# Kernel optimization log

Hardware: AMD Instinct MI355X
Metric: run time of the kernel (lower is better)

## Reference

```python
import jax, jax.numpy as jnp
import numpy as np

NEG = -9e15  # fill value used by the torch module for invalid band locations


def _sliding_window_attention(q, k, v, w, padding_mask):
    """Banded (Longformer-style) attention.
    q, k, v: [B, H, S, d]; padding_mask: [B, S] (nonzero = valid).
    S must be a multiple of 2*w (matches the no-extra-padding path of the
    original module). Returns context [B, H, S, d].
    """
    B, H, S, d = q.shape
    nb = S // w  # number of query blocks of size w
    # Query blocks: [B, H, nb, w, d]
    q_c = q.reshape(B, H, nb, w, d)
    # Each query block attends to a 3w-wide key/value slab (w halo each side).
    idx = (jnp.arange(nb) * w)[:, None] + jnp.arange(3 * w)[None, :]  # [nb, 3w]
    k_pad = jnp.pad(k, ((0, 0), (0, 0), (w, w), (0, 0)))
    v_pad = jnp.pad(v, ((0, 0), (0, 0), (w, w), (0, 0)))
    k_c = k_pad[:, :, idx, :]  # [B, H, nb, 3w, d]
    v_c = v_pad[:, :, idx, :]  # [B, H, nb, 3w, d]
    # Block scores: [B, H, nb, w, 3w]
    scores3 = jnp.einsum('bhnxd,bhnyd->bhnxy', q_c, k_c)
    # Extract the (2w+1)-wide band: query local x, band offset j -> slab col x+j
    x_idx = jnp.arange(w)[:, None]                     # [w, 1]
    j_idx = x_idx + jnp.arange(2 * w + 1)[None, :]     # [w, 2w+1], values in [0, 3w-1]
    band = scores3[..., x_idx, j_idx]                  # [B, H, nb, w, 2w+1]
    # Validity: global key position i - w + j must lie in [0, S) and be unpadded.
    key_pos = jnp.arange(S).reshape(nb, w)[:, :, None] - w + jnp.arange(2 * w + 1)
    valid = (key_pos >= 0) & (key_pos < S)                       # [nb, w, 2w+1]
    kmask = padding_mask[:, jnp.clip(key_pos, 0, S - 1)] != 0    # [B, nb, w, 2w+1]
    m = valid[None, None] & kmask[:, None]                       # [B, H, nb, w, 2w+1]
    band = jnp.where(m, band, NEG)
    # Original scales by sqrt(q.shape[-1]) == sqrt(head_dim)
    attn = jax.nn.softmax(band / jnp.sqrt(jnp.asarray(d, band.dtype)), axis=-1)
    attn = jnp.where(m, attn, 0.0)  # mirrors the explicit softmax_mask zeroing
    # Scatter band back to slab layout and contract with values.
    attn3 = jnp.zeros_like(scores3).at[..., x_idx, j_idx].set(attn)
    ctx = jnp.einsum('bhnxy,bhnyd->bhnxd', attn3, v_c)
    return ctx.reshape(B, H, S, d)


def setup_inputs() -> dict:
    key = jax.random.key(0)
    k0, k1, k2 = jax.random.split(key, 3)
    B, S, D, E = 2, 4096, 1024, 1024
    x = jax.random.normal(k0, (B, S, D), jnp.float32)
    padding_mask = jnp.ones((B, S), jnp.int32)
    # xavier_uniform like the torch _reset_parameters; biases zero
    s_qkv = (6.0 / (D + 3 * E)) ** 0.5
    Wqkv = jax.random.uniform(k1, (3 * E, D), jnp.float32, -s_qkv, s_qkv)
    bqkv = jnp.zeros((3 * E,), jnp.float32)
    s_o = (6.0 / (E + E)) ** 0.5
    Wo = jax.random.uniform(k2, (E, E), jnp.float32, -s_o, s_o)
    bo = jnp.zeros((E,), jnp.float32)
    return {'x': x, 'padding_mask': padding_mask, 'Wqkv': Wqkv, 'bqkv': bqkv,
            'Wo': Wo, 'bo': bo}


def reference(x, padding_mask, Wqkv, bqkv, Wo, bo):
    B, S, D = x.shape
    E = Wo.shape[0]
    H = 16
    hd = E // H
    w = 512 // 2  # window_size // 2
    qkv = (x @ Wqkv.T + bqkv).reshape(B, S, H, 3, hd)
    q = jnp.transpose(qkv[..., 0, :], (0, 2, 1, 3))  # [B, H, S, hd]
    k = jnp.transpose(qkv[..., 1, :], (0, 2, 1, 3))
    v = jnp.transpose(qkv[..., 2, :], (0, 2, 1, 3))
    ctx = _sliding_window_attention(q, k, v, w, padding_mask)
    out = jnp.transpose(ctx, (0, 2, 1, 3)).reshape(B, S, E)
    return out @ Wo.T + bo
```

## Files before the change

kernel.cpp:

```cpp
#include <hip/hip_runtime.h>
#include <hip/hip_bf16.h>
#include <stdint.h>

typedef __attribute__((ext_vector_type(8))) short short8;
typedef __attribute__((ext_vector_type(4))) float f32x4;

#define QSCALE 0.18033688011112042f

__device__ __forceinline__ unsigned short f2bf(float f) {
  unsigned int u = __builtin_bit_cast(unsigned int, f);
  u += 0x7FFFu + ((u >> 16) & 1u);
  return (unsigned short)(u >> 16);
}

__device__ __forceinline__ unsigned short f2bf_fast(float f) {
  __hip_bfloat16 h = __float2bfloat16(f);
  return __builtin_bit_cast(unsigned short, h);
}

__device__ __forceinline__ float exp2_fast(float x) {
  float r; asm("v_exp_f32 %0, %1" : "=v"(r) : "v"(x)); return r;
}

#define GLD_LDS16(gp, lp) \
  __builtin_amdgcn_global_load_lds((const __attribute__((address_space(1))) void*)(gp), \
                                   (__attribute__((address_space(3))) void*)(lp), 16, 0, 0)

__global__ __launch_bounds__(256) void cvt_all_kernel(
    const float* __restrict__ x, const float* __restrict__ Wqkv, const float* __restrict__ Wo,
    unsigned short* __restrict__ xb, unsigned short* __restrict__ Wqkvb,
    unsigned short* __restrict__ Wob) {
  int i = blockIdx.x * 256 + threadIdx.x;
  const float* src; unsigned short* dst; int local; float scale = 1.0f;
  if (i < 1048576) { src = x; dst = xb; local = i; }
  else if (i < 1048576 + 393216) {
    local = i - 1048576; src = Wqkv; dst = Wqkvb;
    int row = (local * 8) >> 10;
    if (((row >> 6) % 3) == 0) scale = QSCALE;
  } else { local = i - 1441792; src = Wo; dst = Wob; }
  const float4* s4 = (const float4*)src;
  float4 a = s4[local * 2], b = s4[local * 2 + 1];
  uint4 o;
  o.x = (unsigned)f2bf(a.x * scale) | ((unsigned)f2bf(a.y * scale) << 16);
  o.y = (unsigned)f2bf(a.z * scale) | ((unsigned)f2bf(a.w * scale) << 16);
  o.z = (unsigned)f2bf(b.x * scale) | ((unsigned)f2bf(b.y * scale) << 16);
  o.w = (unsigned)f2bf(b.z * scale) | ((unsigned)f2bf(b.w * scale) << 16);
  *(uint4*)(dst + (size_t)local * 8) = o;
}

template<int EPI>
__global__ __launch_bounds__(256, 4) void gemm_bt(
    const unsigned short* __restrict__ A, const unsigned short* __restrict__ Bw,
    const float* __restrict__ bias, void* o0, void* o1, void* o2,
    int M, int N, int K, int nbc)
{
  __shared__ __align__(16) unsigned short Asm[128 * 64];
  __shared__ __align__(16) unsigned short Bsm[128 * 64];
  int bid = blockIdx.x;
  int bc = bid % nbc, br = bid / nbc;
  int tid = threadIdx.x;
  int lane = tid & 63, w = tid >> 6;
  int l16 = lane & 15, g = lane >> 4;
  int wr = w >> 1, wc = w & 1;
  f32x4 acc[4][4];
  #pragma unroll
  for (int i = 0; i < 4; i++)
    #pragma unroll
    for (int j = 0; j < 4; j++) acc[i][j] = (f32x4){0.f, 0.f, 0.f, 0.f};

  const int nkt = K >> 6;
  for (int kt = 0; kt < nkt; ++kt) {
    __syncthreads();
    #pragma unroll
    for (int r = 0; r < 4; ++r) {
      int idx = tid + 256 * r;
      int row = idx >> 3, s = idx & 7;
      int gofs = ((s ^ (row & 7)) << 3) + (kt << 6);
      GLD_LDS16(A + (size_t)(br * 128 + row) * K + gofs, &Asm[idx << 3]);
      GLD_LDS16(Bw + (size_t)(bc * 128 + row) * K + gofs, &Bsm[idx << 3]);
    }
    __syncthreads();
    #pragma unroll
    for (int kk = 0; kk < 2; ++kk) {
      short8 af[4], bf[4];
      #pragma unroll
      for (int i = 0; i < 4; i++) {
        int rowa = wr * 64 + i * 16 + l16;
        af[i] = *(const short8*)&Asm[(rowa << 6) + ((((kk << 2) + g) ^ (rowa & 7)) << 3)];
        int rowb = wc * 64 + i * 16 + l16;
        bf[i] = *(const short8*)&Bsm[(rowb << 6) + ((((kk << 2) + g) ^ (rowb & 7)) << 3)];
      }
      #pragma unroll
      for (int i = 0; i < 4; i++)
        #pragma unroll
        for (int j = 0; j < 4; j++)
          acc[i][j] = __builtin_amdgcn_mfma_f32_16x16x32_bf16(af[i], bf[j], acc[i][j], 0, 0, 0);
    }
  }
  #pragma unroll
  for (int i = 0; i < 4; i++) {
    #pragma unroll
    for (int j = 0; j < 4; j++) {
      int n = bc * 128 + wc * 64 + j * 16 + l16;
      int m0 = br * 128 + wr * 64 + i * 16 + g * 4;
      if (EPI == 0) {
        int t = (n >> 6) % 3;
        int hh = n / 192, e = n & 63;
        float bval = bias[n]; if (t == 0) bval *= QSCALE;
        int bb = m0 >> 12, s0 = m0 & 4095;
        if (t == 2) {
          unsigned short p0 = f2bf(acc[i][j][0] + bval);
          unsigned short p1 = f2bf(acc[i][j][1] + bval);
          unsigned short p2 = f2bf(acc[i][j][2] + bval);
          unsigned short p3 = f2bf(acc[i][j][3] + bval);
          uint2 pk;
          pk.x = (unsigned)p0 | ((unsigned)p1 << 16);
          pk.y = (unsigned)p2 | ((unsigned)p3 << 16);
          unsigned short* vt = (unsigned short*)o2;
          *(uint2*)&vt[(((size_t)(bb * 16 + hh) * 64 + e) << 12) + s0] = pk;
        } else {
          unsigned short* dst = (unsigned short*)(t == 0 ? o0 : o1);
          #pragma unroll
          for (int jj = 0; jj < 4; jj++)
            dst[((((size_t)(bb * 16 + hh) << 12) + s0 + jj) << 6) + e] = f2bf(acc[i][j][jj] + bval);
        }
      } else {
        float* o = (float*)o0;
        float bval = bias[n];
        #pragma unroll
        for (int jj = 0; jj < 4; jj++)
          o[(size_t)(m0 + jj) * N + n] = acc[i][j][jj] + bval;
      }
    }
  }
}

__global__ __launch_bounds__(512, 4) void attn_kernel(
    const unsigned short* __restrict__ qb, const unsigned short* __restrict__ kb,
    const unsigned short* __restrict__ vtb, const int* __restrict__ pmask,
    unsigned short* __restrict__ ctxb)
{
  const int S = 4096, HD = 64, WIN = 256;
  const float NEG = -1e38f;
  __shared__ __align__(16) unsigned short Ks[2][64 * 64];
  __shared__ __align__(16) unsigned short Vts[2][64 * 64];
  __shared__ __align__(16) unsigned short Ps[8][16 * 64];

  int bid0 = blockIdx.x;
  int bid = (bid0 & 7) * (gridDim.x >> 3) + (bid0 >> 3);
  int qt = bid & 31;
  int bh = bid >> 5;
  int b = bh >> 4, h = bh & 15;

  const unsigned short* Q  = qb + (size_t)bh * S * HD;
  const unsigned short* Kg = kb + (size_t)bh * S * HD;
  const unsigned short* Vt = vtb + (size_t)bh * HD * S;
  const int* pmrow = pmask + (size_t)b * S;

  int tid = threadIdx.x;
  int lane = tid & 63, w = tid >> 6;
  int l16 = lane & 15, g = lane >> 4;

  int q0 = qt * 128;
  int Q0 = q0 + w * 16;

  short8 qf[2];
  #pragma unroll
  for (int hh = 0; hh < 2; ++hh)
    qf[hh] = *(const short8*)&Q[(size_t)(Q0 + l16) * HD + hh * 32 + g * 8];

  f32x4 ctx[4];
  #pragma unroll
  for (int dt = 0; dt < 4; ++dt) ctx[dt] = (f32x4){0.f, 0.f, 0.f, 0.f};
  float lrun[4] = {0.f, 0.f, 0.f, 0.f};

  int kt0 = (q0 - WIN) >> 6; if (kt0 < 0) kt0 = 0;
  int kt1 = (q0 + 127 + WIN) >> 6; if (kt1 > 63) kt1 = 63;
  int nt = kt1 - kt0 + 1;

#define STAGE(BUF, KT) do {                                                       \
    int kb_ = (KT) * 64;                                                          \
    int row_ = tid >> 3, s_ = tid & 7;                                            \
    int c_ = (s_ ^ (row_ & 7)) << 3;                                              \
    GLD_LDS16(Kg + (size_t)(kb_ + row_) * HD + c_, &Ks[BUF][tid << 3]);           \
    GLD_LDS16(Vt + (size_t)row_ * S + kb_ + c_, &Vts[BUF][tid << 3]);             \
  } while (0)

  STAGE(0, kt0);
  asm volatile("s_waitcnt vmcnt(0)" ::: "memory");
  __syncthreads();

  int cur = 0;
  for (int it = 0; it < nt; ++it) {
    int kbase = (kt0 + it) * 64;
    if (it + 1 < nt) STAGE(cur ^ 1, kt0 + it + 1);

    bool need = (kbase >= Q0 - 319) && (kbase <= Q0 + 271);

    if (need) {
      unsigned long long bm = __ballot(pmrow[kbase + lane] != 0);
      bool allv = (~bm == 0ULL);
      bool full = (kbase >= Q0 - 241) && (kbase <= Q0 + 193);

      f32x4 sc[4];
      __builtin_amdgcn_s_setprio(1);
      #pragma unroll
      for (int k4 = 0; k4 < 4; ++k4) {
        int krow = k4 * 16 + l16;
        f32x4 s = (f32x4){0.f, 0.f, 0.f, 0.f};
        short8 kf0 = *(const short8*)&Ks[cur][(krow << 6) + ((g ^ (l16 & 7)) << 3)];
        s = __builtin_amdgcn_mfma_f32_16x16x32_bf16(qf[0], kf0, s, 0, 0, 0);
        short8 kf1 = *(const short8*)&Ks[cur][(krow << 6) + (((4 + g) ^ (l16 & 7)) << 3)];
        s = __builtin_amdgcn_mfma_f32_16x16x32_bf16(qf[1], kf1, s, 0, 0, 0);
        sc[k4] = s;
      }
      __builtin_amdgcn_s_setprio(0);

      int qbase = Q0 + g * 4;
      if (!full) {
        #pragma unroll
        for (int k4 = 0; k4 < 4; ++k4) {
          int kg = kbase + k4 * 16 + l16;
          #pragma unroll
          for (int jj = 0; jj < 4; ++jj) {
            int dq = kg - (qbase + jj) + WIN;
            sc[k4][jj] = ((unsigned)dq <= 2u * WIN) ? sc[k4][jj] : NEG;
          }
        }
      }
      #pragma unroll
      for (int k4 = 0; k4 < 4; ++k4) {
        int col = k4 * 16 + l16;
        unsigned bit = (unsigned)(bm >> col) & 1u;
        #pragma unroll
        for (int jj = 0; jj < 4; ++jj) {
          float p = exp2_fast(sc[k4][jj]);
          if (!allv) p = bit ? p : 0.f;
          lrun[jj] += p;
          int row = g * 4 + jj;
          Ps[w][(row << 6) + ((((col >> 3) ^ (row & 7)) << 3) | (col & 7))] = f2bf_fast(p);
        }
      }

      asm volatile("s_waitcnt lgkmcnt(0)" ::: "memory");
      __builtin_amdgcn_sched_barrier(0);
      short8 pf0 = *(const short8*)&Ps[w][(l16 << 6) + ((g ^ (l16 & 7)) << 3)];
      short8 pf1 = *(const short8*)&Ps[w][(l16 << 6) + (((4 + g) ^ (l16 & 7)) << 3)];
      __builtin_amdgcn_s_setprio(1);
      #pragma unroll
      for (int dt = 0; dt < 4; ++dt) {
        int drow = dt * 16 + l16;
        short8 vf0 = *(const short8*)&Vts[cur][(drow << 6) + ((g ^ (drow & 7)) << 3)];
        ctx[dt] = __builtin_amdgcn_mfma_f32_16x16x32_bf16(pf0, vf0, ctx[dt], 0, 0, 0);
        short8 vf1 = *(const short8*)&Vts[cur][(drow << 6) + (((4 + g) ^ (drow & 7)) << 3)];
        ctx[dt] = __builtin_amdgcn_mfma_f32_16x16x32_bf16(pf1, vf1, ctx[dt], 0, 0, 0);
      }
      __builtin_amdgcn_s_setprio(0);
    }

    if (it + 1 < nt) {
      asm volatile("s_waitcnt vmcnt(0)" ::: "memory");
      __syncthreads();
      cur ^= 1;
    }
  }
#undef STAGE

  #pragma unroll
  for (int jj = 0; jj < 4; ++jj) {
    float ps = lrun[jj];
    #pragma unroll
    for (int mk = 1; mk < 16; mk <<= 1) ps += __shfl_xor(ps, mk);
    float rc = (ps > 0.f) ? (1.f / ps) : 0.f;
    int qrow = Q0 + g * 4 + jj;
    size_t base = ((size_t)b * S + qrow) * 1024 + h * 64;
    #pragma unroll
    for (int dt = 0; dt < 4; ++dt)
      ctxb[base + dt * 16 + l16] = f2bf(ctx[dt][jj] * rc);
  }
}

extern "C" void kernel_launch(void* const* d_in, const int* in_sizes, int n_in,
                              void* d_out, int out_size, void* d_ws, size_t ws_size,
                              hipStream_t stream) {
  const float* x     = (const float*)d_in[0];
  const int*   pmask = (const int*)d_in[1];
  const float* Wqkv  = (const float*)d_in[2];
  const float* bqkv  = (const float*)d_in[3];
  const float* Wo    = (const float*)d_in[4];
  const float* bo    = (const float*)d_in[5];

  char* wsp = (char*)d_ws;
  unsigned short* xb    = (unsigned short*)(wsp);
  unsigned short* Wqkvb = (unsigned short*)(wsp + (size_t)(16u << 20));
  unsigned short* Wob   = (unsigned short*)(wsp + (size_t)(22u << 20));
  unsigned short* vtb   = (unsigned short*)(wsp + (size_t)(24u << 20));
  unsigned short* ctxb  = (unsigned short*)(wsp + (size_t)(40u << 20));
  unsigned short* qbuf  = (unsigned short*)d_out;
  unsigned short* kbuf  = (unsigned short*)d_out + (size_t)8388608;

  cvt_all_kernel<<<6144, 256, 0, stream>>>(x, Wqkv, Wo, xb, Wqkvb, Wob);

  gemm_bt<0><<<(8192 / 128) * (3072 / 128), 256, 0, stream>>>(
      xb, Wqkvb, bqkv, qbuf, kbuf, vtb, 8192, 3072, 1024, 3072 / 128);

  attn_kernel<<<1024, 512, 0, stream>>>(qbuf, kbuf, vtb, pmask, ctxb);

  gemm_bt<1><<<(8192 / 128) * (1024 / 128), 256, 0, stream>>>(
      ctxb, Wob, bo, d_out, nullptr, nullptr, 8192, 1024, 1024, 1024 / 128);
}
```

Before: 141.7 us.

## Switch attention kernel to 32x32x16 MFMA with 32-row query tiles per wave

Attention now runs 4 waves of 32 query rows each, not 8 waves of 16, and uses 32x32x16 bf16 MFMAs for QK^T and PV instead of 16x16x32. The intent is to raise MFMA efficiency and cut LDS fragment reads per FLOP, since each K/V fragment now serves twice as many query rows. The trade-offs are more accumulator and row-sum registers (16 rows per lane), 256-thread blocks with more staging loads per thread, and coarser band skipping, so more fully masked work is computed per wave.

```diff
diff --git a/kernel.cpp b/kernel.cpp
--- a/kernel.cpp
+++ b/kernel.cpp
@@ -4,6 +4,7 @@
 
 typedef __attribute__((ext_vector_type(8))) short short8;
 typedef __attribute__((ext_vector_type(4))) float f32x4;
+typedef __attribute__((ext_vector_type(16))) float f32x16;
 
 #define QSCALE 0.18033688011112042f
 
@@ -135,16 +136,16 @@
   }
 }
 
-__global__ __launch_bounds__(512, 4) void attn_kernel(
+__global__ __launch_bounds__(256, 3) void attn_kernel(
     const unsigned short* __restrict__ qb, const unsigned short* __restrict__ kb,
     const unsigned short* __restrict__ vtb, const int* __restrict__ pmask,
     unsigned short* __restrict__ ctxb)
 {
-  const int S = 4096, HD = 64, WIN = 256;
+  const int S = 4096, WIN = 256;
   const float NEG = -1e38f;
   __shared__ __align__(16) unsigned short Ks[2][64 * 64];
   __shared__ __align__(16) unsigned short Vts[2][64 * 64];
-  __shared__ __align__(16) unsigned short Ps[8][16 * 64];
+  __shared__ __align__(16) unsigned short Ps[4][32 * 64];
 
   int bid0 = blockIdx.x;
   int bid = (bid0 & 7) * (gridDim.x >> 3) + (bid0 >> 3);
@@ -152,27 +153,27 @@
   int bh = bid >> 5;
   int b = bh >> 4, h = bh & 15;
 
-  const unsigned short* Q  = qb + (size_t)bh * S * HD;
-  const unsigned short* Kg = kb + (size_t)bh * S * HD;
-  const unsigned short* Vt = vtb + (size_t)bh * HD * S;
+  const unsigned short* Q  = qb + (size_t)bh * S * 64;
+  const unsigned short* Kg = kb + (size_t)bh * S * 64;
+  const unsigned short* Vt = vtb + (size_t)bh * 64 * S;
   const int* pmrow = pmask + (size_t)b * S;
 
   int tid = threadIdx.x;
   int lane = tid & 63, w = tid >> 6;
-  int l16 = lane & 15, g = lane >> 4;
+  int l32 = lane & 31, h2 = lane >> 5;
 
   int q0 = qt * 128;
-  int Q0 = q0 + w * 16;
-
-  short8 qf[2];
-  #pragma unroll
-  for (int hh = 0; hh < 2; ++hh)
-    qf[hh] = *(const short8*)&Q[(size_t)(Q0 + l16) * HD + hh * 32 + g * 8];
-
-  f32x4 ctx[4];
-  #pragma unroll
-  for (int dt = 0; dt < 4; ++dt) ctx[dt] = (f32x4){0.f, 0.f, 0.f, 0.f};
-  float lrun[4] = {0.f, 0.f, 0.f, 0.f};
+  int Q0 = q0 + w * 32;
+
+  short8 qf[4];
+  #pragma unroll
+  for (int c = 0; c < 4; ++c)
+    qf[c] = *(const short8*)&Q[(size_t)(Q0 + l32) * 64 + c * 16 + h2 * 8];
+
+  f32x16 ctx0 = (f32x16)(0.f), ctx1 = (f32x16)(0.f);
+  float lrun[16];
+  #pragma unroll
+  for (int r = 0; r < 16; ++r) lrun[r] = 0.f;
 
   int kt0 = (q0 - WIN) >> 6; if (kt0 < 0) kt0 = 0;
   int kt1 = (q0 + 127 + WIN) >> 6; if (kt1 > 63) kt1 = 63;
@@ -180,10 +181,14 @@
 
 #define STAGE(BUF, KT) do {                                                       \
     int kb_ = (KT) * 64;                                                          \
-    int row_ = tid >> 3, s_ = tid & 7;                                            \
-    int c_ = (s_ ^ (row_ & 7)) << 3;                                              \
-    GLD_LDS16(Kg + (size_t)(kb_ + row_) * HD + c_, &Ks[BUF][tid << 3]);           \
-    GLD_LDS16(Vt + (size_t)row_ * S + kb_ + c_, &Vts[BUF][tid << 3]);             \
+    _Pragma("unroll")                                                             \
+    for (int r_ = 0; r_ < 2; ++r_) {                                              \
+      int idx_ = tid + 256 * r_;                                                  \
+      int row_ = idx_ >> 3, s_ = idx_ & 7;                                        \
+      int c_ = (s_ ^ (row_ & 7)) << 3;                                            \
+      GLD_LDS16(Kg + (size_t)(kb_ + row_) * 64 + c_, &Ks[BUF][idx_ << 3]);        \
+      GLD_LDS16(Vt + (size_t)row_ * S + kb_ + c_, &Vts[BUF][idx_ << 3]);          \
+    }                                                                             \
   } while (0)
 
   STAGE(0, kt0);
@@ -195,65 +200,63 @@
     int kbase = (kt0 + it) * 64;
     if (it + 1 < nt) STAGE(cur ^ 1, kt0 + it + 1);
 
-    bool need = (kbase >= Q0 - 319) && (kbase <= Q0 + 271);
-
+    bool need = (kbase >= Q0 - 319) && (kbase <= Q0 + 287);
     if (need) {
       unsigned long long bm = __ballot(pmrow[kbase + lane] != 0);
       bool allv = (~bm == 0ULL);
-      bool full = (kbase >= Q0 - 241) && (kbase <= Q0 + 193);
-
-      f32x4 sc[4];
+      bool full = (kbase >= Q0 - 225) && (kbase <= Q0 + 193);
+
+      f32x16 sc0 = (f32x16)(0.f), sc1 = (f32x16)(0.f);
+      int krow0 = l32, krow1 = 32 + l32;
       __builtin_amdgcn_s_setprio(1);
       #pragma unroll
-      for (int k4 = 0; k4 < 4; ++k4) {
-        int krow = k4 * 16 + l16;
-        f32x4 s = (f32x4){0.f, 0.f, 0.f, 0.f};
-        short8 kf0 = *(const short8*)&Ks[cur][(krow << 6) + ((g ^ (l16 & 7)) << 3)];
-        s = __builtin_amdgcn_mfma_f32_16x16x32_bf16(qf[0], kf0, s, 0, 0, 0);
-        short8 kf1 = *(const short8*)&Ks[cur][(krow << 6) + (((4 + g) ^ (l16 & 7)) << 3)];
-        s = __builtin_amdgcn_mfma_f32_16x16x32_bf16(qf[1], kf1, s, 0, 0, 0);
-        sc[k4] = s;
+      for (int c = 0; c < 4; ++c) {
+        int slot = c * 2 + h2;
+        short8 kf0 = *(const short8*)&Ks[cur][(krow0 << 6) + ((slot ^ (krow0 & 7)) << 3)];
+        sc0 = __builtin_amdgcn_mfma_f32_32x32x16_bf16(qf[c], kf0, sc0, 0, 0, 0);
+        short8 kf1 = *(const short8*)&Ks[cur][(krow1 << 6) + ((slot ^ (krow1 & 7)) << 3)];
+        sc1 = __builtin_amdgcn_mfma_f32_32x32x16_bf16(qf[c], kf1, sc1, 0, 0, 0);
       }
       __builtin_amdgcn_s_setprio(0);
 
-      int qbase = Q0 + g * 4;
+      int col0 = l32, col1 = 32 + l32;
       if (!full) {
         #pragma unroll
-        for (int k4 = 0; k4 < 4; ++k4) {
-          int kg = kbase + k4 * 16 + l16;
-          #pragma unroll
-          for (int jj = 0; jj < 4; ++jj) {
-            int dq = kg - (qbase + jj) + WIN;
-            sc[k4][jj] = ((unsigned)dq <= 2u * WIN) ? sc[k4][jj] : NEG;
-          }
+        for (int r = 0; r < 16; ++r) {
+          int row = (r & 3) + 8 * (r >> 2) + 4 * h2;
+          int d0 = kbase + col0 - (Q0 + row) + WIN;
+          sc0[r] = ((unsigned)d0 <= 2u * WIN) ? sc0[r] : NEG;
+          int d1 = kbase + col1 - (Q0 + row) + WIN;
+          sc1[r] = ((unsigned)d1 <= 2u * WIN) ? sc1[r] : NEG;
         }
       }
-      #pragma unroll
-      for (int k4 = 0; k4 < 4; ++k4) {
-        int col = k4 * 16 + l16;
-        unsigned bit = (unsigned)(bm >> col) & 1u;
-        #pragma unroll
-        for (int jj = 0; jj < 4; ++jj) {
-          float p = exp2_fast(sc[k4][jj]);
-          if (!allv) p = bit ? p : 0.f;
-          lrun[jj] += p;
-          int row = g * 4 + jj;
-          Ps[w][(row << 6) + ((((col >> 3) ^ (row & 7)) << 3) | (col & 7))] = f2bf_fast(p);
-        }
+      unsigned bit0 = (unsigned)(bm >> col0) & 1u;
+      unsigned bit1 = (unsigned)(bm >> col1) & 1u;
+      #pragma unroll
+      for (int r = 0; r < 16; ++r) {
+        int row = (r & 3) + 8 * (r >> 2) + 4 * h2;
+        float p0 = exp2_fast(sc0[r]);
+        float p1 = exp2_fast(sc1[r]);
+        if (!allv) { p0 = bit0 ? p0 : 0.f; p1 = bit1 ? p1 : 0.f; }
+        lrun[r] += p0 + p1;
+        int rb = (row << 6), rx = (row & 7);
+        Ps[w][rb + ((((col0 >> 3) ^ rx) << 3) | (col0 & 7))] = f2bf_fast(p0);
+        Ps[w][rb + ((((col1 >> 3) ^ rx) << 3) | (col1 & 7))] = f2bf_fast(p1);
       }
 
       asm volatile("s_waitcnt lgkmcnt(0)" ::: "memory");
       __builtin_amdgcn_sched_barrier(0);
-      short8 pf0 = *(const short8*)&Ps[w][(l16 << 6) + ((g ^ (l16 & 7)) << 3)];
-      short8 pf1 = *(const short8*)&Ps[w][(l16 << 6) + (((4 + g) ^ (l16 & 7)) << 3)];
+
       __builtin_amdgcn_s_setprio(1);
       #pragma unroll
-      for (int dt = 0; dt < 4; ++dt) {
-        int drow = dt * 16 + l16;
-        short8 vf0 = *(const short8*)&Vts[cur][(drow << 6) + ((g ^ (drow & 7)) << 3)];
-        ctx[dt] = __builtin_amdgcn_mfma_f32_16x16x32_bf16(pf0, vf0, ctx[dt], 0, 0, 0);
-        short8 vf1 = *(const short8*)&Vts[cur][(drow << 6) + (((4 + g) ^ (drow & 7)) << 3)];
-        ctx[dt] = __builtin_amdgcn_mfma_f32_16x16x32_bf16(pf1, vf1, ctx[dt], 0, 0, 0);
+      for (int c = 0; c < 4; ++c) {
+        int slot = c * 2 + h2;
+        short8 pf = *(const short8*)&Ps[w][(l32 << 6) + ((slot ^ (l32 & 7)) << 3)];
+        int dr0 = l32, dr1 = 32 + l32;
+        short8 vf0 = *(const short8*)&Vts[cur][(dr0 << 6) + ((slot ^ (dr0 & 7)) << 3)];
+        ctx0 = __builtin_amdgcn_mfma_f32_32x32x16_bf16(pf, vf0, ctx0, 0, 0, 0);
+        short8 vf1 = *(const short8*)&Vts[cur][(dr1 << 6) + ((slot ^ (dr1 & 7)) << 3)];
+        ctx1 = __builtin_amdgcn_mfma_f32_32x32x16_bf16(pf, vf1, ctx1, 0, 0, 0);
       }
       __builtin_amdgcn_s_setprio(0);
     }
@@ -267,16 +270,19 @@
 #undef STAGE
 
   #pragma unroll
-  for (int jj = 0; jj < 4; ++jj) {
-    float ps = lrun[jj];
-    #pragma unroll
-    for (int mk = 1; mk < 16; mk <<= 1) ps += __shfl_xor(ps, mk);
-    float rc = (ps > 0.f) ? (1.f / ps) : 0.f;
-    int qrow = Q0 + g * 4 + jj;
+  for (int r = 0; r < 16; ++r) {
+    float ps = lrun[r];
+    #pragma unroll
+    for (int mk = 1; mk < 32; mk <<= 1) ps += __shfl_xor(ps, mk);
+    lrun[r] = (ps > 0.f) ? (1.f / ps) : 0.f;
+  }
+  #pragma unroll
+  for (int r = 0; r < 16; ++r) {
+    int row = (r & 3) + 8 * (r >> 2) + 4 * h2;
+    int qrow = Q0 + row;
     size_t base = ((size_t)b * S + qrow) * 1024 + h * 64;
-    #pragma unroll
-    for (int dt = 0; dt < 4; ++dt)
-      ctxb[base + dt * 16 + l16] = f2bf(ctx[dt][jj] * rc);
+    ctxb[base + l32]      = f2bf(ctx0[r] * lrun[r]);
+    ctxb[base + 32 + l32] = f2bf(ctx1[r] * lrun[r]);
   }
 }
 
@@ -304,7 +310,7 @@
   gemm_bt<0><<<(8192 / 128) * (3072 / 128), 256, 0, stream>>>(
       xb, Wqkvb, bqkv, qbuf, kbuf, vtb, 8192, 3072, 1024, 3072 / 128);
 
-  attn_kernel<<<1024, 512, 0, stream>>>(qbuf, kbuf, vtb, pmask, ctxb);
+  attn_kernel<<<1024, 256, 0, stream>>>(qbuf, kbuf, vtb, pmask, ctxb);
 
   gemm_bt<1><<<(8192 / 128) * (1024 / 128), 256, 0, stream>>>(
       ctxb, Wob, bo, d_out, nullptr, nullptr, 8192, 1024, 1024, 1024 / 128);
```

Result: slower. 157.2 us (+10.9%).

## Give each attention wave two query sub-tiles to reuse K/V fragments

Applied to the files above, without the earlier changes.

The attention kernel moves from 8 waves per block with 16 query rows each to 4 waves per block with 32 query rows each (two 16-row sub-tiles). Each K and V fragment read from LDS now feeds two MFMAs, which halves LDS reads per FLOP. The masking and exp pass is fused into the QK loop per k4 chunk, and K/V staging is split across two loads per thread. The cost is more registers per wave and fewer waves per block to hide latency, and the wider query span means some tiles are computed that one sub-tile does not need.

```diff
diff --git a/kernel.cpp b/kernel.cpp
--- a/kernel.cpp
+++ b/kernel.cpp
@@ -135,16 +135,16 @@
   }
 }
 
-__global__ __launch_bounds__(512, 4) void attn_kernel(
+__global__ __launch_bounds__(256, 4) void attn_kernel(
     const unsigned short* __restrict__ qb, const unsigned short* __restrict__ kb,
     const unsigned short* __restrict__ vtb, const int* __restrict__ pmask,
     unsigned short* __restrict__ ctxb)
 {
-  const int S = 4096, HD = 64, WIN = 256;
+  const int S = 4096, WIN = 256;
   const float NEG = -1e38f;
   __shared__ __align__(16) unsigned short Ks[2][64 * 64];
   __shared__ __align__(16) unsigned short Vts[2][64 * 64];
-  __shared__ __align__(16) unsigned short Ps[8][16 * 64];
+  __shared__ __align__(16) unsigned short Ps[4][2][16 * 64];
 
   int bid0 = blockIdx.x;
   int bid = (bid0 & 7) * (gridDim.x >> 3) + (bid0 >> 3);
@@ -152,9 +152,9 @@
   int bh = bid >> 5;
   int b = bh >> 4, h = bh & 15;
 
-  const unsigned short* Q  = qb + (size_t)bh * S * HD;
-  const unsigned short* Kg = kb + (size_t)bh * S * HD;
-  const unsigned short* Vt = vtb + (size_t)bh * HD * S;
+  const unsigned short* Q  = qb + (size_t)bh * S * 64;
+  const unsigned short* Kg = kb + (size_t)bh * S * 64;
+  const unsigned short* Vt = vtb + (size_t)bh * 64 * S;
   const int* pmrow = pmask + (size_t)b * S;
 
   int tid = threadIdx.x;
@@ -162,17 +162,21 @@
   int l16 = lane & 15, g = lane >> 4;
 
   int q0 = qt * 128;
-  int Q0 = q0 + w * 16;
-
-  short8 qf[2];
-  #pragma unroll
-  for (int hh = 0; hh < 2; ++hh)
-    qf[hh] = *(const short8*)&Q[(size_t)(Q0 + l16) * HD + hh * 32 + g * 8];
-
-  f32x4 ctx[4];
-  #pragma unroll
-  for (int dt = 0; dt < 4; ++dt) ctx[dt] = (f32x4){0.f, 0.f, 0.f, 0.f};
-  float lrun[4] = {0.f, 0.f, 0.f, 0.f};
+  int Q0 = q0 + w * 32;
+
+  short8 qf[2][2];
+  #pragma unroll
+  for (int qs = 0; qs < 2; ++qs)
+    #pragma unroll
+    for (int hh = 0; hh < 2; ++hh)
+      qf[qs][hh] = *(const short8*)&Q[(size_t)(Q0 + qs * 16 + l16) * 64 + hh * 32 + g * 8];
+
+  f32x4 ctx[2][4];
+  #pragma unroll
+  for (int qs = 0; qs < 2; ++qs)
+    #pragma unroll
+    for (int dt = 0; dt < 4; ++dt) ctx[qs][dt] = (f32x4){0.f, 0.f, 0.f, 0.f};
+  float lrun[2][4] = {{0.f,0.f,0.f,0.f},{0.f,0.f,0.f,0.f}};
 
   int kt0 = (q0 - WIN) >> 6; if (kt0 < 0) kt0 = 0;
   int kt1 = (q0 + 127 + WIN) >> 6; if (kt1 > 63) kt1 = 63;
@@ -180,10 +184,14 @@
 
 #define STAGE(BUF, KT) do {                                                       \
     int kb_ = (KT) * 64;                                                          \
-    int row_ = tid >> 3, s_ = tid & 7;                                            \
-    int c_ = (s_ ^ (row_ & 7)) << 3;                                              \
-    GLD_LDS16(Kg + (size_t)(kb_ + row_) * HD + c_, &Ks[BUF][tid << 3]);           \
-    GLD_LDS16(Vt + (size_t)row_ * S + kb_ + c_, &Vts[BUF][tid << 3]);             \
+    _Pragma("unroll")                                                             \
+    for (int r_ = 0; r_ < 2; ++r_) {                                              \
+      int idx_ = tid + 256 * r_;                                                  \
+      int row_ = idx_ >> 3, s_ = idx_ & 7;                                        \
+      int c_ = (s_ ^ (row_ & 7)) << 3;                                            \
+      GLD_LDS16(Kg + (size_t)(kb_ + row_) * 64 + c_, &Ks[BUF][idx_ << 3]);        \
+      GLD_LDS16(Vt + (size_t)row_ * S + kb_ + c_, &Vts[BUF][idx_ << 3]);          \
+    }                                                                             \
   } while (0)
 
   STAGE(0, kt0);
@@ -195,65 +203,76 @@
     int kbase = (kt0 + it) * 64;
     if (it + 1 < nt) STAGE(cur ^ 1, kt0 + it + 1);
 
-    bool need = (kbase >= Q0 - 319) && (kbase <= Q0 + 271);
-
+    bool need = (kbase >= Q0 - 319) && (kbase <= Q0 + 287);
     if (need) {
       unsigned long long bm = __ballot(pmrow[kbase + lane] != 0);
       bool allv = (~bm == 0ULL);
-      bool full = (kbase >= Q0 - 241) && (kbase <= Q0 + 193);
-
-      f32x4 sc[4];
+      bool full0 = (kbase >= Q0 - 241) && (kbase <= Q0 + 193);
+      bool full1 = (kbase >= Q0 - 225) && (kbase <= Q0 + 209);
+
       __builtin_amdgcn_s_setprio(1);
       #pragma unroll
       for (int k4 = 0; k4 < 4; ++k4) {
         int krow = k4 * 16 + l16;
-        f32x4 s = (f32x4){0.f, 0.f, 0.f, 0.f};
         short8 kf0 = *(const short8*)&Ks[cur][(krow << 6) + ((g ^ (l16 & 7)) << 3)];
-        s = __builtin_amdgcn_mfma_f32_16x16x32_bf16(qf[0], kf0, s, 0, 0, 0);
+        f32x4 s0 = __builtin_amdgcn_mfma_f32_16x16x32_bf16(qf[0][0], kf0,
+                     (f32x4){0.f, 0.f, 0.f, 0.f}, 0, 0, 0);
+        f32x4 s1 = __builtin_amdgcn_mfma_f32_16x16x32_bf16(qf[1][0], kf0,
+                     (f32x4){0.f, 0.f, 0.f, 0.f}, 0, 0, 0);
         short8 kf1 = *(const short8*)&Ks[cur][(krow << 6) + (((4 + g) ^ (l16 & 7)) << 3)];
-        s = __builtin_amdgcn_mfma_f32_16x16x32_bf16(qf[1], kf1, s, 0, 0, 0);
-        sc[k4] = s;
-      }
-      __builtin_amdgcn_s_setprio(0);
-
-      int qbase = Q0 + g * 4;
-      if (!full) {
+        s0 = __builtin_amdgcn_mfma_f32_16x16x32_bf16(qf[0][1], kf1, s0, 0, 0, 0);
+        s1 = __builtin_amdgcn_mfma_f32_16x16x32_bf16(qf[1][1], kf1, s1, 0, 0, 0);
+
+        int col = k4 * 16 + l16;
+        int kg = kbase + col;
+        unsigned bit = (unsigned)(bm >> col) & 1u;
         #pragma unroll
-        for (int k4 = 0; k4 < 4; ++k4) {
-          int kg = kbase + k4 * 16 + l16;
-          #pragma unroll
-          for (int jj = 0; jj < 4; ++jj) {
-            int dq = kg - (qbase + jj) + WIN;
-            sc[k4][jj] = ((unsigned)dq <= 2u * WIN) ? sc[k4][jj] : NEG;
+        for (int jj = 0; jj < 4; ++jj) {
+          int row = g * 4 + jj;
+          int pofs = (row << 6) + ((((col >> 3) ^ (row & 7)) << 3) | (col & 7));
+          {
+            float sv = s0[jj];
+            if (!full0) {
+              int dq = kg - (Q0 + row) + WIN;
+              sv = ((unsigned)dq <= 2u * WIN) ? sv : NEG;
+            }
+            float p = exp2_fast(sv);
+            if (!allv) p = bit ? p : 0.f;
+            lrun[0][jj] += p;
+            Ps[w][0][pofs] = f2bf_fast(p);
+          }
+          {
+            float sv = s1[jj];
+            if (!full1) {
+              int dq = kg - (Q0 + 16 + row) + WIN;
+              sv = ((unsigned)dq <= 2u * WIN) ? sv : NEG;
+            }
+            float p = exp2_fast(sv);
+            if (!allv) p = bit ? p : 0.f;
+            lrun[1][jj] += p;
+            Ps[w][1][pofs] = f2bf_fast(p);
           }
         }
       }
-      #pragma unroll
-      for (int k4 = 0; k4 < 4; ++k4) {
-        int col = k4 * 16 + l16;
-        unsigned bit = (unsigned)(bm >> col) & 1u;
-        #pragma unroll
-        for (int jj = 0; jj < 4; ++jj) {
-          float p = exp2_fast(sc[k4][jj]);
-          if (!allv) p = bit ? p : 0.f;
-          lrun[jj] += p;
-          int row = g * 4 + jj;
-          Ps[w][(row << 6) + ((((col >> 3) ^ (row & 7)) << 3) | (col & 7))] = f2bf_fast(p);
-        }
-      }
+      __builtin_amdgcn_s_setprio(0);
 
       asm volatile("s_waitcnt lgkmcnt(0)" ::: "memory");
       __builtin_amdgcn_sched_barrier(0);
-      short8 pf0 = *(const short8*)&Ps[w][(l16 << 6) + ((g ^ (l16 & 7)) << 3)];
-      short8 pf1 = *(const short8*)&Ps[w][(l16 << 6) + (((4 + g) ^ (l16 & 7)) << 3)];
+
+      short8 pf00 = *(const short8*)&Ps[w][0][(l16 << 6) + ((g ^ (l16 & 7)) << 3)];
+      short8 pf01 = *(const short8*)&Ps[w][0][(l16 << 6) + (((4 + g) ^ (l16 & 7)) << 3)];
+      short8 pf10 = *(const short8*)&Ps[w][1][(l16 << 6) + ((g ^ (l16 & 7)) << 3)];
+      short8 pf11 = *(const short8*)&Ps[w][1][(l16 << 6) + (((4 + g) ^ (l16 & 7)) << 3)];
       __builtin_amdgcn_s_setprio(1);
       #pragma unroll
       for (int dt = 0; dt < 4; ++dt) {
         int drow = dt * 16 + l16;
         short8 vf0 = *(const short8*)&Vts[cur][(drow << 6) + ((g ^ (drow & 7)) << 3)];
-        ctx[dt] = __builtin_amdgcn_mfma_f32_16x16x32_bf16(pf0, vf0, ctx[dt], 0, 0, 0);
+        ctx[0][dt] = __builtin_amdgcn_mfma_f32_16x16x32_bf16(pf00, vf0, ctx[0][dt], 0, 0, 0);
+        ctx[1][dt] = __builtin_amdgcn_mfma_f32_16x16x32_bf16(pf10, vf0, ctx[1][dt], 0, 0, 0);
         short8 vf1 = *(const short8*)&Vts[cur][(drow << 6) + (((4 + g) ^ (drow & 7)) << 3)];
-        ctx[dt] = __builtin_amdgcn_mfma_f32_16x16x32_bf16(pf1, vf1, ctx[dt], 0, 0, 0);
+        ctx[0][dt] = __builtin_amdgcn_mfma_f32_16x16x32_bf16(pf01, vf1, ctx[0][dt], 0, 0, 0);
+        ctx[1][dt] = __builtin_amdgcn_mfma_f32_16x16x32_bf16(pf11, vf1, ctx[1][dt], 0, 0, 0);
       }
       __builtin_amdgcn_s_setprio(0);
     }
@@ -267,16 +286,19 @@
 #undef STAGE
 
   #pragma unroll
-  for (int jj = 0; jj < 4; ++jj) {
-    float ps = lrun[jj];
-    #pragma unroll
-    for (int mk = 1; mk < 16; mk <<= 1) ps += __shfl_xor(ps, mk);
-    float rc = (ps > 0.f) ? (1.f / ps) : 0.f;
-    int qrow = Q0 + g * 4 + jj;
-    size_t base = ((size_t)b * S + qrow) * 1024 + h * 64;
-    #pragma unroll
-    for (int dt = 0; dt < 4; ++dt)
-      ctxb[base + dt * 16 + l16] = f2bf(ctx[dt][jj] * rc);
+  for (int qs = 0; qs < 2; ++qs) {
+    #pragma unroll
+    for (int jj = 0; jj < 4; ++jj) {
+      float ps = lrun[qs][jj];
+      #pragma unroll
+      for (int mk = 1; mk < 16; mk <<= 1) ps += __shfl_xor(ps, mk);
+      float rc = (ps > 0.f) ? (1.f / ps) : 0.f;
+      int qrow = Q0 + qs * 16 + g * 4 + jj;
+      size_t base = ((size_t)b * S + qrow) * 1024 + h * 64;
+      #pragma unroll
+      for (int dt = 0; dt < 4; ++dt)
+        ctxb[base + dt * 16 + l16] = f2bf(ctx[qs][dt][jj] * rc);
+    }
   }
 }
 
@@ -304,7 +326,7 @@
   gemm_bt<0><<<(8192 / 128) * (3072 / 128), 256, 0, stream>>>(
       xb, Wqkvb, bqkv, qbuf, kbuf, vtb, 8192, 3072, 1024, 3072 / 128);
 
-  attn_kernel<<<1024, 512, 0, stream>>>(qbuf, kbuf, vtb, pmask, ctxb);
+  attn_kernel<<<1024, 256, 0, stream>>>(qbuf, kbuf, vtb, pmask, ctxb);
 
   gemm_bt<1><<<(8192 / 128) * (1024 / 128), 256, 0, stream>>>(
       ctxb, Wob, bo, d_out, nullptr, nullptr, 8192, 1024, 1024, 1024 / 128);
```

Result: slower. 153.1 us (+8.0%).
